# Kernel optimization log

Hardware: AMD Instinct MI355X
Metric: run time of the kernel (lower is better)

Reference implementation:

```python
import jax, jax.numpy as jnp
import numpy as np

L = 2; B = 16; H = 56; W = 56; N = H * W; D = 256
HEADS = 8; HD = 32; INNER = HEADS * HD
WIN = 7; WIN2 = WIN * WIN; NWH = H // WIN; NWW = W // WIN; NW = NWH * NWW
DISP = WIN // 2; FF = 4 * D; CPB = 512; EPS = 1e-5


def _shift_masks():
    d = DISP
    ul = np.zeros((WIN2, WIN2), np.float32)
    ul[-d * WIN:, :-d * WIN] = -np.inf
    ul[:-d * WIN, -d * WIN:] = -np.inf
    lr = np.zeros((WIN, WIN, WIN, WIN), np.float32)
    lr[:, -d:, :, :-d] = -np.inf
    lr[:, :-d, :, -d:] = -np.inf
    return jnp.asarray(ul), jnp.asarray(lr.reshape(WIN2, WIN2))

MASK_UL, MASK_LR = _shift_masks()

_idx = np.array([[i, j] for i in range(WIN) for j in range(WIN)], np.float32)
_rel = _idx[None, :, :] - _idx[:, None, :]  # (49,49,2) relative distances
REL = jnp.asarray((np.sign(_rel) * np.log1p(np.abs(_rel))).reshape(WIN2 * WIN2, 2))


def _ln(x, g, b):
    m = x.mean(-1, keepdims=True)
    v = ((x - m) ** 2).mean(-1, keepdims=True)
    return (x - m) / jnp.sqrt(v + EPS) * g + b


def _l2norm(t):
    return t / jnp.maximum(jnp.linalg.norm(t, axis=-1, keepdims=True), 1e-12)


def _window_attn(xm, qkv_w, tau, cw1, cb1, cw2, cb2, ow, ob, shifted):
    if shifted:
        xm = jnp.roll(xm, (-DISP, -DISP), (1, 2))
    qkv = xm @ qkv_w  # (B,H,W,3*INNER), no bias
    q, k, v = jnp.split(qkv, 3, axis=-1)

    def towin(t):  # (B,H,W,INNER) -> (B,heads,nw,win2,hd)
        t = t.reshape(B, NWH, WIN, NWW, WIN, HEADS, HD)
        return t.transpose(0, 5, 1, 3, 2, 4, 6).reshape(B, HEADS, NW, WIN2, HD)

    q, k, v = towin(q), towin(k), towin(v)
    # cosine-similarity attention
    dots = jnp.einsum('bhwid,bhwjd->bhwij', _l2norm(q), _l2norm(k))
    dots = dots / jnp.clip(tau, 0.01, None)[None, :, None, None, None]
    # continuous position bias MLP: 2 -> CPB -> heads
    cpb = (jax.nn.relu(REL @ cw1 + cb1) @ cw2 + cb2).reshape(WIN2, WIN2, HEADS)
    dots = dots + cpb.transpose(2, 0, 1)[None, :, None]
    if shifted:
        dots = dots.at[:, :, -NWW:].add(MASK_UL)
        dots = dots.at[:, :, NWW - 1::NWW].add(MASK_LR)
    attn = jax.nn.softmax(dots, -1)
    out = jnp.einsum('bhwij,bhwjd->bhwid', attn, v)
    out = out.reshape(B, HEADS, NWH, NWW, WIN, WIN, HD)
    out = out.transpose(0, 2, 4, 3, 5, 1, 6).reshape(B, H, W, INNER)
    out = out @ ow + ob
    if shifted:
        out = jnp.roll(out, (DISP, DISP), (1, 2))
    return out


def _forward(x, spe, qkv_w, tau, cw1, cb1, cw2, cb2, ow, ob, ln1_g, ln1_b,
             fw1, fb1, fw2, fb2, ln2_g, ln2_b, norm_g, norm_b):
    xm = (x + spe).reshape(B, H, W, D)
    for i in range(L):
        shifted = (i % 2 == 1)
        a = _window_attn(xm, qkv_w[i], tau[i], cw1[i], cb1[i], cw2[i], cb2[i],
                         ow[i], ob[i], shifted)
        xm = _ln(a, ln1_g[i], ln1_b[i]) + xm  # Residual(PostNorm(attn))
        f = jax.nn.gelu(xm @ fw1[i] + fb1[i], approximate=False) @ fw2[i] + fb2[i]
        xm = _ln(f, ln2_g[i], ln2_b[i]) + xm  # Residual(PostNorm(mlp))
    return _ln(xm, norm_g, norm_b).reshape(B, N, D)


def setup_inputs():
    key = jax.random.key(0)
    ks = jax.random.split(key, 10)
    rn = lambda k, shp, s: jax.random.normal(k, shp, jnp.float32) * s
    return {
        'x': rn(ks[0], (B, N, D), 1.0),
        'spatial_position_embedding': rn(ks[1], (B, N, D), 0.02),
        'qkv_w': rn(ks[2], (L, D, 3 * INNER), 0.02),
        'tau': jnp.ones((L, HEADS), jnp.float32),
        'cw1': rn(ks[3], (L, 2, CPB), 0.1),
        'cb1': jnp.zeros((L, CPB), jnp.float32),
        'cw2': rn(ks[4], (L, CPB, HEADS), 0.05),
        'cb2': jnp.zeros((L, HEADS), jnp.float32),
        'ow': rn(ks[5], (L, INNER, D), 0.02),
        'ob': jnp.zeros((L, D), jnp.float32),
        'ln1_g': jnp.ones((L, D), jnp.float32),
        'ln1_b': jnp.zeros((L, D), jnp.float32),
        'fw1': rn(ks[6], (L, D, FF), 0.02),
        'fb1': jnp.zeros((L, FF), jnp.float32),
        'fw2': rn(ks[7], (L, FF, D), 0.02),
        'fb2': jnp.zeros((L, D), jnp.float32),
        'ln2_g': jnp.ones((L, D), jnp.float32),
        'ln2_b': jnp.zeros((L, D), jnp.float32),
        'norm_g': jnp.ones((D,), jnp.float32),
        'norm_b': jnp.zeros((D,), jnp.float32),
    }


def reference(x, spatial_position_embedding, qkv_w, tau, cw1, cb1, cw2, cb2, ow, ob,
              ln1_g, ln1_b, fw1, fb1, fw2, fb2, ln2_g, ln2_b, norm_g, norm_b):
    return _forward(x, spatial_position_embedding, qkv_w, tau, cw1, cb1, cw2, cb2,
                    ow, ob, ln1_g, ln1_b, fw1, fb1, fw2, fb2, ln2_g, ln2_b,
                    norm_g, norm_b)
```

## Files before the change

### kernel.cpp

```cpp
#include <hip/hip_runtime.h>
#include <hip/hip_bf16.h>
#include <math.h>

typedef short    short8  __attribute__((ext_vector_type(8)));
typedef float    floatx4 __attribute__((ext_vector_type(4)));

__device__ __forceinline__ float b2f(unsigned short u) {
    union { float f; unsigned int i; } v; v.i = ((unsigned int)u) << 16; return v.f;
}
__device__ __forceinline__ unsigned short f2b(float f) {
    union { float f; unsigned int i; } v; v.f = f;
    unsigned int b = v.i;
    return (unsigned short)((b + 0x7FFFu + ((b >> 16) & 1u)) >> 16);
}
__device__ __forceinline__ float rd(const void* p, long i, int f) {
    return f ? ((const float*)p)[i] : b2f(((const unsigned short*)p)[i]);
}
__device__ __forceinline__ float fgelu(float x) {
    float u = 0.7978845608f * x * (1.f + 0.044715f * x * x);
    float e = __expf(-2.f * fabsf(u));
    float th = 1.f - 2.f * e / (1.f + e);
    th = (u < 0.f) ? -th : th;
    return 0.5f * x * (1.f + th);
}
__device__ __forceinline__ void gl_lds16(const unsigned short* g, unsigned short* l) {
    __builtin_amdgcn_global_load_lds(
        (const __attribute__((address_space(1))) void*)g,
        (__attribute__((address_space(3))) void*)l, 16, 0, 0);
}

#define NTOK_ 50176

__global__ __launch_bounds__(256) void k_detect(const unsigned short* __restrict__ x,
                                                int* __restrict__ flag) {
    __shared__ int cnt;
    if (threadIdx.x == 0) cnt = 0;
    __syncthreads();
    unsigned short v = x[threadIdx.x];
    int e = (v >> 7) & 0xFF;
    if (e >= 0x90) atomicAdd(&cnt, 1);
    __syncthreads();
    if (threadIdx.x == 0) *flag = (cnt >= 8) ? 1 : 0;
}

__global__ __launch_bounds__(256) void k_add_spe(const void* __restrict__ x,
                                                 const void* __restrict__ spe,
                                                 float* __restrict__ xm,
                                                 unsigned short* __restrict__ xb,
                                                 const int* __restrict__ flagp) {
    const int f = *flagp;
    long i = ((long)blockIdx.x * 256 + threadIdx.x) * 4;
    float4 o;
    if (f) {
        float4 a = *(const float4*)((const float*)x + i);
        float4 b = *(const float4*)((const float*)spe + i);
        o.x = a.x + b.x; o.y = a.y + b.y; o.z = a.z + b.z; o.w = a.w + b.w;
    } else {
        ushort4 a = *(const ushort4*)((const unsigned short*)x + i);
        ushort4 b = *(const ushort4*)((const unsigned short*)spe + i);
        o.x = b2f(a.x) + b2f(b.x); o.y = b2f(a.y) + b2f(b.y);
        o.z = b2f(a.z) + b2f(b.z); o.w = b2f(a.w) + b2f(b.w);
    }
    *(float4*)(xm + i) = o;
    if (xb) {
        ushort4 h; h.x = f2b(o.x); h.y = f2b(o.y); h.z = f2b(o.z); h.w = f2b(o.w);
        *(ushort4*)(xb + i) = h;
    }
}

__global__ __launch_bounds__(256) void k_transpose(const void* __restrict__ in, long ioff,
                                                   unsigned short* __restrict__ out,
                                                   int K, int N,
                                                   const int* __restrict__ flagp) {
    __shared__ unsigned short tile[32][33];
    const int f = *flagp;
    int n0 = blockIdx.x * 32, k0 = blockIdx.y * 32;
    int tx = threadIdx.x & 31, ty = threadIdx.x >> 5;
#pragma unroll
    for (int i = 0; i < 4; i++) {
        int k = k0 + ty + i * 8;
        long idx = ioff + (long)k * N + n0 + tx;
        unsigned short v = f ? f2b(((const float*)in)[idx])
                             : ((const unsigned short*)in)[idx];
        tile[ty + i * 8][tx] = v;
    }
    __syncthreads();
#pragma unroll
    for (int i = 0; i < 4; i++) {
        int n = n0 + ty + i * 8;
        out[(long)n * K + k0 + tx] = tile[tx][ty + i * 8];
    }
}

__global__ __launch_bounds__(512) void k_cpb(const void* __restrict__ cw1,
                                             const void* __restrict__ cb1,
                                             const void* __restrict__ cw2,
                                             const void* __restrict__ cb2,
                                             float* __restrict__ cpb,
                                             const int* __restrict__ flagp) {
    const int f = *flagp;
    int p = blockIdx.x;
    int l = blockIdx.y;
    int t = threadIdx.x;
    int i = p / 49, j = p - i * 49;
    int yi = i / 7, xi = i - yi * 7, yj = j / 7, xj = j - yj * 7;
    float dy = (float)(yj - yi), dx = (float)(xj - xi);
    float sy = (dy > 0.f) ? 1.f : ((dy < 0.f) ? -1.f : 0.f);
    float sx = (dx > 0.f) ? 1.f : ((dx < 0.f) ? -1.f : 0.f);
    float r0 = sy * log1pf(fabsf(dy));
    float r1 = sx * log1pf(fabsf(dx));
    float h = r0 * rd(cw1, l * 1024 + t, f) + r1 * rd(cw1, l * 1024 + 512 + t, f)
            + rd(cb1, l * 512 + t, f);
    h = fmaxf(h, 0.f);
    __shared__ float red[512];
    for (int hh = 0; hh < 8; hh++) {
        red[t] = h * rd(cw2, (long)(l * 512 + t) * 8 + hh, f);
        __syncthreads();
        for (int s = 256; s > 0; s >>= 1) {
            if (t < s) red[t] += red[t + s];
            __syncthreads();
        }
        if (t == 0) cpb[((long)l * 8 + hh) * 2401 + p] = red[0] + rd(cb2, l * 8 + hh, f);
        __syncthreads();
    }
}

__global__ __launch_bounds__(256) void k_cast_roll(const float* __restrict__ xmg,
                                                   unsigned short* __restrict__ xb, int shift) {
    int gid = blockIdx.x * 256 + threadIdx.x;
    int c4 = (gid & 63) * 4;
    int t = gid >> 6;
    int x = t % 56; int t2 = t / 56;
    int y = t2 % 56;
    int b = t2 / 56;
    int ys = y + shift; if (ys >= 56) ys -= 56;
    int xs = x + shift; if (xs >= 56) xs -= 56;
    float4 v = *(const float4*)(xmg + (((long)b * 3136 + ys * 56 + xs) * 256 + c4));
    ushort4 o; o.x = f2b(v.x); o.y = f2b(v.y); o.z = f2b(v.z); o.w = f2b(v.w);
    *(ushort4*)(xb + ((long)t * 256 + c4)) = o;
}

__global__ __launch_bounds__(256) void gemm_bt(const unsigned short* __restrict__ A,
                                               const unsigned short* __restrict__ Bt,
                                               const void* __restrict__ bias, long boff,
                                               void* __restrict__ Cp,
                                               int M, int N, int K, int flags,
                                               const int* __restrict__ flagp) {
    __shared__ __align__(16) unsigned short smem[16896];
    unsigned short* As = smem;
    unsigned short* Bs = smem + 4096;
    const int f = *flagp;
    const int tid = threadIdx.x;
    const int lane = tid & 63;
    const int wave = tid >> 6;
    const int wrow = (wave >> 1) * 64;
    const int wcol = (wave & 1) * 64;
    const int bn = blockIdx.x, bm = blockIdx.y;

    floatx4 acc[4][4] = {};

    const int trow = tid >> 2;
    const int tseg = (tid & 3) * 8;
    const unsigned short* Ag = A + (long)(bm * 128 + trow) * K + tseg;
    const unsigned short* Bg = Bt + (long)(bn * 128 + trow) * K + tseg;
    const long rstep = (long)64 * K;
    unsigned short* Asw = As + wave * 512;
    unsigned short* Bsw = Bs + wave * 512;

    const int q = lane >> 4;
    const int mrow = lane & 15;

    for (int k0 = 0; k0 < K; k0 += 32) {
        __syncthreads();
        gl_lds16(Ag + k0, Asw);
        gl_lds16(Ag + k0 + rstep, Asw + 2048);
        gl_lds16(Bg + k0, Bsw);
        gl_lds16(Bg + k0 + rstep, Bsw + 2048);
        __syncthreads();

        short8 af_[4], bf_[4];
#pragma unroll
        for (int mt = 0; mt < 4; mt++)
            af_[mt] = *(const short8*)(As + (wrow + mt * 16 + mrow) * 32 + q * 8);
#pragma unroll
        for (int nt = 0; nt < 4; nt++)
            bf_[nt] = *(const short8*)(Bs + (wcol + nt * 16 + mrow) * 32 + q * 8);
#pragma unroll
        for (int mt = 0; mt < 4; mt++)
#pragma unroll
            for (int nt = 0; nt < 4; nt++)
                acc[mt][nt] = __builtin_amdgcn_mfma_f32_16x16x32_bf16(af_[mt], bf_[nt], acc[mt][nt], 0, 0, 0);
    }

    __syncthreads();

    if (flags & 4) {
        unsigned short* T = smem;
#pragma unroll
        for (int nt = 0; nt < 4; nt++) {
            int col = wcol + nt * 16 + mrow;
            float bv = (flags & 1) ? rd(bias, boff + bn * 128 + col, f) : 0.f;
#pragma unroll
            for (int mt = 0; mt < 4; mt++) {
                int row0 = wrow + mt * 16 + q * 4;
#pragma unroll
                for (int r = 0; r < 4; r++) {
                    float v = acc[mt][nt][r] + bv;
                    if (flags & 2) v = fgelu(v);
                    T[(row0 + r) * 132 + col] = f2b(v);
                }
            }
        }
        __syncthreads();
        unsigned short* Cu = (unsigned short*)Cp;
        int row = tid >> 4;
        int col8 = (tid & 15) * 8;
#pragma unroll
        for (int p = 0; p < 8; p++) {
            int rr = p * 16 + row;
            *(uint4*)(Cu + (long)(bm * 128 + rr) * N + bn * 128 + col8) =
                *(const uint4*)(T + rr * 132 + col8);
        }
    } else {
        float* Tf = (float*)smem;
        float* Cf = (float*)Cp;
        float bvc[4];
#pragma unroll
        for (int nt = 0; nt < 4; nt++)
            bvc[nt] = (flags & 1) ? rd(bias, boff + bn * 128 + wcol + nt * 16 + mrow, f) : 0.f;
        int row = tid >> 5;
        int col4 = (tid & 31) * 4;
#pragma unroll
        for (int half = 0; half < 2; half++) {
            if (half) __syncthreads();
            if (wrow == half * 64) {
#pragma unroll
                for (int nt = 0; nt < 4; nt++) {
                    int col = wcol + nt * 16 + mrow;
#pragma unroll
                    for (int mt = 0; mt < 4; mt++) {
                        int lrow0 = mt * 16 + q * 4;
#pragma unroll
                        for (int r = 0; r < 4; r++) {
                            float v = acc[mt][nt][r] + bvc[nt];
                            if (flags & 2) v = fgelu(v);
                            Tf[(lrow0 + r) * 132 + col] = v;
                        }
                    }
                }
            }
            __syncthreads();
#pragma unroll
            for (int p = 0; p < 8; p++) {
                int rr = p * 8 + row;
                *(float4*)(Cf + (long)(bm * 128 + half * 64 + rr) * N + bn * 128 + col4) =
                    *(const float4*)(Tf + rr * 132 + col4);
            }
        }
    }
}

__global__ __launch_bounds__(256) void gemm_ln(const unsigned short* __restrict__ A,
                                               const unsigned short* __restrict__ Bt,
                                               const void* __restrict__ bias, long boff,
                                               const void* __restrict__ g, long goff,
                                               const void* __restrict__ bb, long b2off,
                                               float* __restrict__ xm,
                                               unsigned short* __restrict__ xb,
                                               int K, int xbmode,
                                               const int* __restrict__ flagp) {
    __shared__ __align__(16) unsigned short smem[17152];
    __shared__ float pp[4][64][2];
    unsigned short* As = smem;
    unsigned short* Bs = smem + 2048;
    const int f = *flagp;
    const int tid = threadIdx.x;
    const int lane = tid & 63;
    const int wv = tid >> 6;
    const int wcol = wv * 64;
    const int bm = blockIdx.x;

    floatx4 acc[4][4] = {};
    const int trow = tid >> 2;
    const int tseg = (tid & 3) * 8;
    const unsigned short* Ag = A + (long)(bm * 64 + trow) * K + tseg;
    const unsigned short* Bg = Bt + (long)trow * K + tseg;
    const long rstep = (long)64 * K;
    unsigned short* Asw = As + wv * 512;
    unsigned short* Bsw = Bs + wv * 512;
    const int q = lane >> 4;
    const int c = lane & 15;

    for (int k0 = 0; k0 < K; k0 += 32) {
        __syncthreads();
        gl_lds16(Ag + k0, Asw);
        gl_lds16(Bg + k0, Bsw);
        gl_lds16(Bg + k0 + rstep, Bsw + 2048);
        gl_lds16(Bg + k0 + 2 * rstep, Bsw + 4096);
        gl_lds16(Bg + k0 + 3 * rstep, Bsw + 6144);
        __syncthreads();

        short8 af_[4], bf_[4];
#pragma unroll
        for (int mt = 0; mt < 4; mt++)
            af_[mt] = *(const short8*)(As + (mt * 16 + c) * 32 + q * 8);
#pragma unroll
        for (int nt = 0; nt < 4; nt++)
            bf_[nt] = *(const short8*)(Bs + (wcol + nt * 16 + c) * 32 + q * 8);
#pragma unroll
        for (int mt = 0; mt < 4; mt++)
#pragma unroll
            for (int nt = 0; nt < 4; nt++)
                acc[mt][nt] = __builtin_amdgcn_mfma_f32_16x16x32_bf16(af_[mt], bf_[nt], acc[mt][nt], 0, 0, 0);
    }
    __syncthreads();

    float bv[4];
#pragma unroll
    for (int nt = 0; nt < 4; nt++)
        bv[nt] = rd(bias, boff + wcol + nt * 16 + c, f);
#pragma unroll
    for (int mt = 0; mt < 4; mt++) {
#pragma unroll
        for (int r = 0; r < 4; r++) {
            float s1 = 0.f, s2 = 0.f;
#pragma unroll
            for (int nt = 0; nt < 4; nt++) {
                float v = acc[mt][nt][r] + bv[nt];
                s1 += v; s2 += v * v;
            }
            s1 += __shfl_xor(s1, 1); s2 += __shfl_xor(s2, 1);
            s1 += __shfl_xor(s1, 2); s2 += __shfl_xor(s2, 2);
            s1 += __shfl_xor(s1, 4); s2 += __shfl_xor(s2, 4);
            s1 += __shfl_xor(s1, 8); s2 += __shfl_xor(s2, 8);
            if (c == 0) {
                pp[wv][mt * 16 + q * 4 + r][0] = s1;
                pp[wv][mt * 16 + q * 4 + r][1] = s2;
            }
        }
    }

    const int c0 = lane * 4;
    float4 gv, bbv;
    gv.x = rd(g, goff + c0 + 0, f); gv.y = rd(g, goff + c0 + 1, f);
    gv.z = rd(g, goff + c0 + 2, f); gv.w = rd(g, goff + c0 + 3, f);
    bbv.x = rd(bb, b2off + c0 + 0, f); bbv.y = rd(bb, b2off + c0 + 1, f);
    bbv.z = rd(bb, b2off + c0 + 2, f); bbv.w = rd(bb, b2off + c0 + 3, f);
    __syncthreads();

    float* Tf = (float*)smem;
#pragma unroll
    for (int half = 0; half < 2; half++) {
        if (half) __syncthreads();
#pragma unroll
        for (int mt2 = 0; mt2 < 2; mt2++) {
            int mt = half * 2 + mt2;
#pragma unroll
            for (int nt = 0; nt < 4; nt++)
#pragma unroll
                for (int r = 0; r < 4; r++)
                    Tf[(mt2 * 16 + q * 4 + r) * 268 + wcol + nt * 16 + c] = acc[mt][nt][r] + bv[nt];
        }
        __syncthreads();
#pragma unroll
        for (int it = 0; it < 8; it++) {
            int lr = wv * 8 + it;
            int row = half * 32 + lr;
            float sum = pp[0][row][0] + pp[1][row][0] + pp[2][row][0] + pp[3][row][0];
            float ssq = pp[0][row][1] + pp[1][row][1] + pp[2][row][1] + pp[3][row][1];
            float mean = sum * (1.f / 256.f);
            float var = ssq * (1.f / 256.f) - mean * mean;
            float rstd = rsqrtf(fmaxf(var, 0.f) + 1e-5f);
            long tok = (long)(bm * 64 + row);
            long grow = tok * 256;
            float4 t = *(const float4*)(Tf + lr * 268 + c0);
            float4 xv = *(const float4*)(xm + grow + c0);
            float4 o;
            o.x = (t.x - mean) * rstd * gv.x + bbv.x + xv.x;
            o.y = (t.y - mean) * rstd * gv.y + bbv.y + xv.y;
            o.z = (t.z - mean) * rstd * gv.z + bbv.z + xv.z;
            o.w = (t.w - mean) * rstd * gv.w + bbv.w + xv.w;
            *(float4*)(xm + grow + c0) = o;
            if (xbmode) {
                long xg = grow;
                if (xbmode == 2) {
                    int bi = (int)(tok / 3136); int r2 = (int)(tok - (long)bi * 3136);
                    int y = r2 / 56; int x = r2 - y * 56;
                    y = (y >= 3) ? y - 3 : y + 53;
                    x = (x >= 3) ? x - 3 : x + 53;
                    xg = ((long)bi * 3136 + y * 56 + x) * 256;
                }
                ushort4 hb; hb.x = f2b(o.x); hb.y = f2b(o.y); hb.z = f2b(o.z); hb.w = f2b(o.w);
                *(ushort4*)(xb + xg + c0) = hb;
            }
        }
    }
}

__global__ __launch_bounds__(256) void k_attn(const unsigned short* __restrict__ qkv,
                                              const float* __restrict__ cpb,
                                              const void* __restrict__ tau, long toff,
                                              unsigned short* __restrict__ out,
                                              int shifted,
                                              const int* __restrict__ flagp) {
    __shared__ __align__(16) unsigned short Pbuf[4][64 * 72];
    __shared__ __align__(16) unsigned short Vt[4][32 * 72];
    __shared__ float inq_s[4][64], ink_s[4][64];

    const int f = *flagp;
    const int tid = threadIdx.x;
    const int wv = tid >> 6;
    const int lane = tid & 63;
    const int h = blockIdx.x * 4 + wv;
    const int w = blockIdx.y, b = blockIdx.z;
    const int wy = w >> 3, wx = w & 7;
    const int q = lane >> 4;
    const int c = lane & 15;

    short8 qa[4], kb[4];
    float sqv[4], skv[4];
#pragma unroll
    for (int mt = 0; mt < 4; mt++) {
        int i = mt * 16 + c; if (i > 48) i = 48;
        int py = i / 7, px = i - py * 7;
        long base = (((long)b * 56 + wy * 7 + py) * 56 + wx * 7 + px) * 768 + h * 32 + q * 8;
        qa[mt] = *(const short8*)(qkv + base);
        kb[mt] = *(const short8*)(qkv + base + 256);
        float sq = 0.f, sk = 0.f;
#pragma unroll
        for (int e = 0; e < 8; e++) {
            float a = b2f((unsigned short)qa[mt][e]); sq += a * a;
            float k2 = b2f((unsigned short)kb[mt][e]); sk += k2 * k2;
        }
        sqv[mt] = sq; skv[mt] = sk;
    }
#pragma unroll
    for (int mt = 0; mt < 4; mt++) {
        float sq = sqv[mt]; sq += __shfl_xor(sq, 16); sq += __shfl_xor(sq, 32);
        float sk = skv[mt]; sk += __shfl_xor(sk, 16); sk += __shfl_xor(sk, 32);
        if (q == 0) {
            inq_s[wv][mt * 16 + c] = 1.f / fmaxf(sqrtf(sq), 1e-12f);
            ink_s[wv][mt * 16 + c] = 1.f / fmaxf(sqrtf(sk), 1e-12f);
        }
    }

    floatx4 acc[4][4] = {};
#pragma unroll
    for (int mt = 0; mt < 4; mt++)
#pragma unroll
        for (int nt = 0; nt < 4; nt++)
            acc[mt][nt] = __builtin_amdgcn_mfma_f32_16x16x32_bf16(qa[mt], kb[nt], acc[mt][nt], 0, 0, 0);

#pragma unroll
    for (int z = lane; z < 576; z += 64)
        *(uint2*)(&Vt[wv][z * 4]) = make_uint2(0u, 0u);
    if (lane < 49) {
        int py = lane / 7, px = lane - py * 7;
        long base = (((long)b * 56 + wy * 7 + py) * 56 + wx * 7 + px) * 768 + h * 32 + 512;
#pragma unroll
        for (int dd = 0; dd < 32; dd += 8) {
            ushort4 v0 = *(const ushort4*)(qkv + base + dd);
            ushort4 v1 = *(const ushort4*)(qkv + base + dd + 4);
            Vt[wv][(dd + 0) * 72 + lane] = v0.x;
            Vt[wv][(dd + 1) * 72 + lane] = v0.y;
            Vt[wv][(dd + 2) * 72 + lane] = v0.z;
            Vt[wv][(dd + 3) * 72 + lane] = v0.w;
            Vt[wv][(dd + 4) * 72 + lane] = v1.x;
            Vt[wv][(dd + 5) * 72 + lane] = v1.y;
            Vt[wv][(dd + 6) * 72 + lane] = v1.z;
            Vt[wv][(dd + 7) * 72 + lane] = v1.w;
        }
    }

    float scale = 1.f / fmaxf(rd(tau, toff + h, f), 0.01f);
#pragma unroll
    for (int mt = 0; mt < 4; mt++) {
#pragma unroll
        for (int r = 0; r < 4; r++) {
            int i = mt * 16 + q * 4 + r;
            int ci = (i < 49) ? i : 48;
            int pyi = ci / 7, pxi = ci - pyi * 7;
            float qi = inq_s[wv][ci] * scale;
            float vals[4];
#pragma unroll
            for (int nt = 0; nt < 4; nt++) {
                int j = nt * 16 + c;
                if (j < 49) {
                    float v = acc[mt][nt][r] * qi * ink_s[wv][j]
                            + cpb[h * 2401 + ci * 49 + j];
                    if (shifted) {
                        int pyj = j / 7, pxj = j - pyj * 7;
                        if (wy == 7 && ((pyi >= 4) != (pyj >= 4))) v = -1e30f;
                        if (wx == 7 && ((pxi >= 4) != (pxj >= 4))) v = -1e30f;
                    }
                    vals[nt] = v;
                } else vals[nt] = -1e30f;
            }
            float m = fmaxf(fmaxf(vals[0], vals[1]), fmaxf(vals[2], vals[3]));
            m = fmaxf(m, __shfl_xor(m, 1)); m = fmaxf(m, __shfl_xor(m, 2));
            m = fmaxf(m, __shfl_xor(m, 4)); m = fmaxf(m, __shfl_xor(m, 8));
            float s = 0.f;
#pragma unroll
            for (int nt = 0; nt < 4; nt++) { vals[nt] = __expf(vals[nt] - m); s += vals[nt]; }
            s += __shfl_xor(s, 1); s += __shfl_xor(s, 2);
            s += __shfl_xor(s, 4); s += __shfl_xor(s, 8);
            float rinv = 1.f / s;
#pragma unroll
            for (int nt = 0; nt < 4; nt++)
                Pbuf[wv][i * 72 + nt * 16 + c] = f2b(vals[nt] * rinv);
        }
    }

    floatx4 accO[4][2] = {};
#pragma unroll
    for (int ks = 0; ks < 2; ks++) {
        short8 pa[4], vb[2];
#pragma unroll
        for (int mt = 0; mt < 4; mt++)
            pa[mt] = *(const short8*)(&Pbuf[wv][(mt * 16 + c) * 72 + ks * 32 + q * 8]);
#pragma unroll
        for (int nt = 0; nt < 2; nt++)
            vb[nt] = *(const short8*)(&Vt[wv][(nt * 16 + c) * 72 + ks * 32 + q * 8]);
#pragma unroll
        for (int mt = 0; mt < 4; mt++)
#pragma unroll
            for (int nt = 0; nt < 2; nt++)
                accO[mt][nt] = __builtin_amdgcn_mfma_f32_16x16x32_bf16(pa[mt], vb[nt], accO[mt][nt], 0, 0, 0);
    }

    int sh = shifted ? 3 : 0;
#pragma unroll
    for (int mt = 0; mt < 4; mt++) {
#pragma unroll
        for (int r = 0; r < 4; r++) {
            int i = mt * 16 + q * 4 + r;
            if (i < 49) {
                int py = i / 7, px = i - py * 7;
                int yo = wy * 7 + py + sh; if (yo >= 56) yo -= 56;
                int xo = wx * 7 + px + sh; if (xo >= 56) xo -= 56;
                long ob = (((long)b * 56 + yo) * 56 + xo) * 256 + h * 32;
                out[ob + c]      = f2b(accO[mt][0][r]);
                out[ob + 16 + c] = f2b(accO[mt][1][r]);
            }
        }
    }
}

__global__ __launch_bounds__(256) void k_final(const float* __restrict__ xm,
                                               const void* __restrict__ g,
                                               const void* __restrict__ bb,
                                               void* __restrict__ out,
                                               const int* __restrict__ flagp) {
    const int f = *flagp;
    int t = blockIdx.x, c = threadIdx.x;
    long off = (long)t * 256 + c;
    float v = xm[off];
    __shared__ float red[256];
    red[c] = v; __syncthreads();
#pragma unroll
    for (int s = 128; s > 0; s >>= 1) {
        if (c < s) red[c] += red[c + s];
        __syncthreads();
    }
    float mean = red[0] * (1.f / 256.f);
    __syncthreads();
    float d = v - mean;
    red[c] = d * d; __syncthreads();
#pragma unroll
    for (int s = 128; s > 0; s >>= 1) {
        if (c < s) red[c] += red[c + s];
        __syncthreads();
    }
    float var = red[0] * (1.f / 256.f);
    float ln = d * rsqrtf(var + 1e-5f) * rd(g, c, f) + rd(bb, c, f);
    if (f) ((float*)out)[off] = ln;
    else   ((unsigned short*)out)[off] = f2b(ln);
}

extern "C" void kernel_launch(void* const* d_in, const int* in_sizes, int n_in,
                              void* d_out, int out_size, void* d_ws, size_t ws_size,
                              hipStream_t stream) {
    char* ws = (char*)d_ws;
    float*          xm    = (float*)(ws + 0);
    unsigned short* wt    = (unsigned short*)(ws + 51380224);
    float*          cpb   = (float*)(ws + 54525952);
    int*            flagp = (int*)(ws + 54679616);
    const size_t DYN = 54680576;

    long Mg = NTOK_; int G = 1;
    while (G <= 8) {
        Mg = NTOK_ / G;
        if (DYN + (size_t)Mg * 2560 <= ws_size) break;
        G <<= 1;
    }
    if (G > 8) { G = 8; Mg = NTOK_ / 8; }
    const int NB = 16 / G;
    const bool fused = (G == 1);

    unsigned short* xb   = (unsigned short*)(ws + DYN);
    unsigned short* qkvb = (unsigned short*)(ws + DYN + Mg * 512);
    unsigned short* hid  = (unsigned short*)(ws + DYN + Mg * 512);

    k_detect<<<1, 256, 0, stream>>>((const unsigned short*)d_in[0], flagp);

    for (int l = 0; l < 2; l++) {
        unsigned short* base = wt + (long)l * 786432;
        k_transpose<<<dim3(24, 8), 256, 0, stream>>>(d_in[2],  (long)l * 196608, base,          256, 768,  flagp);
        k_transpose<<<dim3(8, 8),  256, 0, stream>>>(d_in[8],  (long)l * 65536,  base + 196608, 256, 256,  flagp);
        k_transpose<<<dim3(32, 8), 256, 0, stream>>>(d_in[12], (long)l * 262144, base + 262144, 256, 1024, flagp);
        k_transpose<<<dim3(8, 32), 256, 0, stream>>>(d_in[14], (long)l * 262144, base + 524288, 1024, 256, flagp);
    }
    k_cpb<<<dim3(2401, 2), 512, 0, stream>>>(d_in[4], d_in[5], d_in[6], d_in[7], cpb, flagp);
    k_add_spe<<<dim3(12544), 256, 0, stream>>>(d_in[0], d_in[1], xm,
                                               fused ? xb : (unsigned short*)nullptr, flagp);

    for (int l = 0; l < 2; l++) {
        int sh = (l & 1) ? 3 : 0;
        unsigned short* base = wt + (long)l * 786432;
        for (int g = 0; g < G; g++) {
            long m0 = (long)g * Mg;
            if (!fused)
                k_cast_roll<<<dim3(Mg / 4), 256, 0, stream>>>(xm + m0 * 256, xb, sh);
            gemm_bt<<<dim3(6, Mg / 128), 256, 0, stream>>>(xb, base, nullptr, 0, qkvb,
                                                           (int)Mg, 768, 256, 4, flagp);
            k_attn<<<dim3(2, 64, NB), 256, 0, stream>>>(qkvb, cpb + (long)l * 19208,
                                                        d_in[3], (long)l * 8, xb, (l & 1), flagp);
            gemm_ln<<<dim3(Mg / 64), 256, 0, stream>>>(xb, base + 196608, d_in[9], (long)l * 256,
                                                       d_in[10], (long)l * 256, d_in[11], (long)l * 256,
                                                       xm + m0 * 256, xb, 256, 1, flagp);
            gemm_bt<<<dim3(8, Mg / 128), 256, 0, stream>>>(xb, base + 262144, d_in[13], (long)l * 1024,
                                                           hid, (int)Mg, 1024, 256, 1 | 2 | 4, flagp);
            int xbm = fused ? ((l == 0) ? 2 : 0) : 1;
            gemm_ln<<<dim3(Mg / 64), 256, 0, stream>>>(hid, base + 524288, d_in[15], (long)l * 256,
                                                       d_in[16], (long)l * 256, d_in[17], (long)l * 256,
                                                       xm + m0 * 256, xb, 1024, xbm, flagp);
        }
    }
    k_final<<<dim3(NTOK_), 256, 0, stream>>>(xm, d_in[18], d_in[19], d_out, flagp);
}
```

Measured before the change: 965.5 us.

## Double-buffer LDS tiles in GEMM kernels to overlap loads with MFMA

Both the plain GEMM and the GEMM+LayerNorm kernels now use two LDS stages. The next K-slice is issued via global-to-LDS loads while MFMAs run on the current slice, which cuts one barrier per iteration. The aim is to hide global memory latency behind compute. In exchange, LDS use grows, which can lower occupancy for gemm_ln, and correctness now depends on the single barrier ordering reads and writes to each buffer.

```diff
diff --git a/kernel.cpp b/kernel.cpp
--- a/kernel.cpp
+++ b/kernel.cpp
@@ -147,8 +147,6 @@
                                                int M, int N, int K, int flags,
                                                const int* __restrict__ flagp) {
     __shared__ __align__(16) unsigned short smem[16896];
-    unsigned short* As = smem;
-    unsigned short* Bs = smem + 4096;
     const int f = *flagp;
     const int tid = threadIdx.x;
     const int lane = tid & 63;
@@ -164,32 +162,42 @@
     const unsigned short* Ag = A + (long)(bm * 128 + trow) * K + tseg;
     const unsigned short* Bg = Bt + (long)(bn * 128 + trow) * K + tseg;
     const long rstep = (long)64 * K;
-    unsigned short* Asw = As + wave * 512;
-    unsigned short* Bsw = Bs + wave * 512;
+    const int wbase = wave * 512;
 
     const int q = lane >> 4;
     const int mrow = lane & 15;
 
-    for (int k0 = 0; k0 < K; k0 += 32) {
-        __syncthreads();
-        gl_lds16(Ag + k0, Asw);
-        gl_lds16(Ag + k0 + rstep, Asw + 2048);
-        gl_lds16(Bg + k0, Bsw);
-        gl_lds16(Bg + k0 + rstep, Bsw + 2048);
-        __syncthreads();
-
+    gl_lds16(Ag, smem + wbase);
+    gl_lds16(Ag + rstep, smem + 2048 + wbase);
+    gl_lds16(Bg, smem + 4096 + wbase);
+    gl_lds16(Bg + rstep, smem + 6144 + wbase);
+    __syncthreads();
+
+    int cur = 0;
+    for (int k0 = 32; ; k0 += 32, cur ^= 1) {
+        if (k0 < K) {
+            unsigned short* Sn = smem + (cur ^ 1) * 8192;
+            gl_lds16(Ag + k0, Sn + wbase);
+            gl_lds16(Ag + k0 + rstep, Sn + 2048 + wbase);
+            gl_lds16(Bg + k0, Sn + 4096 + wbase);
+            gl_lds16(Bg + k0 + rstep, Sn + 6144 + wbase);
+        }
+        const unsigned short* Ac = smem + cur * 8192;
+        const unsigned short* Bc = Ac + 4096;
         short8 af_[4], bf_[4];
 #pragma unroll
         for (int mt = 0; mt < 4; mt++)
-            af_[mt] = *(const short8*)(As + (wrow + mt * 16 + mrow) * 32 + q * 8);
+            af_[mt] = *(const short8*)(Ac + (wrow + mt * 16 + mrow) * 32 + q * 8);
 #pragma unroll
         for (int nt = 0; nt < 4; nt++)
-            bf_[nt] = *(const short8*)(Bs + (wcol + nt * 16 + mrow) * 32 + q * 8);
+            bf_[nt] = *(const short8*)(Bc + (wcol + nt * 16 + mrow) * 32 + q * 8);
 #pragma unroll
         for (int mt = 0; mt < 4; mt++)
 #pragma unroll
             for (int nt = 0; nt < 4; nt++)
                 acc[mt][nt] = __builtin_amdgcn_mfma_f32_16x16x32_bf16(af_[mt], bf_[nt], acc[mt][nt], 0, 0, 0);
+        if (k0 >= K) break;
+        __syncthreads();
     }
 
     __syncthreads();
@@ -269,10 +277,8 @@
                                                unsigned short* __restrict__ xb,
                                                int K, int xbmode,
                                                const int* __restrict__ flagp) {
-    __shared__ __align__(16) unsigned short smem[17152];
+    __shared__ __align__(16) unsigned short smem[20480];
     __shared__ float pp[4][64][2];
-    unsigned short* As = smem;
-    unsigned short* Bs = smem + 2048;
     const int f = *flagp;
     const int tid = threadIdx.x;
     const int lane = tid & 63;
@@ -286,32 +292,43 @@
     const unsigned short* Ag = A + (long)(bm * 64 + trow) * K + tseg;
     const unsigned short* Bg = Bt + (long)trow * K + tseg;
     const long rstep = (long)64 * K;
-    unsigned short* Asw = As + wv * 512;
-    unsigned short* Bsw = Bs + wv * 512;
+    const int wbase = wv * 512;
     const int q = lane >> 4;
     const int c = lane & 15;
 
-    for (int k0 = 0; k0 < K; k0 += 32) {
-        __syncthreads();
-        gl_lds16(Ag + k0, Asw);
-        gl_lds16(Bg + k0, Bsw);
-        gl_lds16(Bg + k0 + rstep, Bsw + 2048);
-        gl_lds16(Bg + k0 + 2 * rstep, Bsw + 4096);
-        gl_lds16(Bg + k0 + 3 * rstep, Bsw + 6144);
-        __syncthreads();
-
+    gl_lds16(Ag, smem + wbase);
+    gl_lds16(Bg, smem + 2048 + wbase);
+    gl_lds16(Bg + rstep, smem + 4096 + wbase);
+    gl_lds16(Bg + 2 * rstep, smem + 6144 + wbase);
+    gl_lds16(Bg + 3 * rstep, smem + 8192 + wbase);
+    __syncthreads();
+
+    int cur = 0;
+    for (int k0 = 32; ; k0 += 32, cur ^= 1) {
+        if (k0 < K) {
+            unsigned short* Sn = smem + (cur ^ 1) * 10240;
+            gl_lds16(Ag + k0, Sn + wbase);
+            gl_lds16(Bg + k0, Sn + 2048 + wbase);
+            gl_lds16(Bg + k0 + rstep, Sn + 4096 + wbase);
+            gl_lds16(Bg + k0 + 2 * rstep, Sn + 6144 + wbase);
+            gl_lds16(Bg + k0 + 3 * rstep, Sn + 8192 + wbase);
+        }
+        const unsigned short* Ac = smem + cur * 10240;
+        const unsigned short* Bc = Ac + 2048;
         short8 af_[4], bf_[4];
 #pragma unroll
         for (int mt = 0; mt < 4; mt++)
-            af_[mt] = *(const short8*)(As + (mt * 16 + c) * 32 + q * 8);
+            af_[mt] = *(const short8*)(Ac + (mt * 16 + c) * 32 + q * 8);
 #pragma unroll
         for (int nt = 0; nt < 4; nt++)
-            bf_[nt] = *(const short8*)(Bs + (wcol + nt * 16 + c) * 32 + q * 8);
+            bf_[nt] = *(const short8*)(Bc + (wcol + nt * 16 + c) * 32 + q * 8);
 #pragma unroll
         for (int mt = 0; mt < 4; mt++)
 #pragma unroll
             for (int nt = 0; nt < 4; nt++)
                 acc[mt][nt] = __builtin_amdgcn_mfma_f32_16x16x32_bf16(af_[mt], bf_[nt], acc[mt][nt], 0, 0, 0);
+        if (k0 >= K) break;
+        __syncthreads();
     }
     __syncthreads();
 
```

Result: slower. 1.030 ms (+6.7%).
